# Optimization experiments

Hardware: AMD Instinct MI355X
Metric: run time of the kernel (lower is better)

The kernel has to match this reference:

```python
import jax, jax.numpy as jnp
import numpy as np

D_MODEL = 1024
N_HEADS = 16
D_FF = 512  # FeedForward default d_ff=512 (not overridden in EncoderLayer)
EPS = 1e-6


def _norm(x, alpha, bias):
    # Custom NormLayer: mean + UNBIASED variance (torch.var default, N-1 denom)
    mean = jnp.mean(x, axis=-1, keepdims=True)
    n = x.shape[-1]
    var = jnp.sum((x - mean) ** 2, axis=-1, keepdims=True) / (n - 1)
    return alpha * (x - mean) / jnp.sqrt(var + EPS) + bias


def setup_inputs() -> dict:
    key = jax.random.key(0)
    ks = jax.random.split(key, 12)
    s = 1.0 / np.sqrt(D_MODEL)
    inp = {
        "x": jax.random.normal(ks[0], (2, 2048, D_MODEL), dtype=jnp.float32),
        "Wq": jax.random.uniform(ks[1], (D_MODEL, D_MODEL), jnp.float32, -s, s),
        "bq": jnp.zeros((D_MODEL,), jnp.float32),
        "Wk": jax.random.uniform(ks[2], (D_MODEL, D_MODEL), jnp.float32, -s, s),
        "bk": jnp.zeros((D_MODEL,), jnp.float32),
        "Wv": jax.random.uniform(ks[3], (D_MODEL, D_MODEL), jnp.float32, -s, s),
        "bv": jnp.zeros((D_MODEL,), jnp.float32),
        "Wo": jax.random.uniform(ks[4], (D_MODEL, D_MODEL), jnp.float32, -s, s),
        "bo": jnp.zeros((D_MODEL,), jnp.float32),
        "alpha1": jnp.ones((D_MODEL,), jnp.float32),
        "beta1": jnp.zeros((D_MODEL,), jnp.float32),
        "alpha2": jnp.ones((D_MODEL,), jnp.float32),
        "beta2": jnp.zeros((D_MODEL,), jnp.float32),
        "W1": jax.random.uniform(ks[5], (D_MODEL, D_FF), jnp.float32, -s, s),
        "b1": jnp.zeros((D_FF,), jnp.float32),
        "W2": jax.random.uniform(ks[6], (D_FF, D_MODEL), jnp.float32, -1.0 / np.sqrt(D_FF), 1.0 / np.sqrt(D_FF)),
        "b2": jnp.zeros((D_MODEL,), jnp.float32),
    }
    return inp


def reference(x, Wq, bq, Wk, bk, Wv, bv, Wo, bo, alpha1, beta1, alpha2, beta2, W1, b1, W2, b2):
    B, S, D = x.shape
    H = N_HEADS
    dh = D // H
    # norm_1 applied to x, result feeds BOTH attention and the residual
    x = _norm(x, alpha1, beta1)
    # multihead attention (dropout = identity in eval)
    q = (x @ Wq + bq).reshape(B, S, H, dh)
    k = (x @ Wk + bk).reshape(B, S, H, dh)
    v = (x @ Wv + bv).reshape(B, S, H, dh)
    scores = jnp.einsum("bqhd,bkhd->bhqk", q, k) / jnp.sqrt(jnp.asarray(dh, x.dtype))
    attn = jax.nn.softmax(scores, axis=-1)
    o = jnp.einsum("bhqk,bkhd->bqhd", attn, v).reshape(B, S, D)
    o = o @ Wo + bo
    x = x + o
    # FFN on norm_2(x)
    h = _norm(x, alpha2, beta2)
    h = jax.nn.relu(h @ W1 + b1) @ W2 + b2
    return x + h
```

## Files before the change

### kernel.cpp

```cpp
#include <hip/hip_runtime.h>

typedef __bf16 bf16;
typedef __bf16 bf16x4 __attribute__((ext_vector_type(4)));
typedef __bf16 bf16x8 __attribute__((ext_vector_type(8)));
typedef float f32x4 __attribute__((ext_vector_type(4)));

#define D_MODEL 1024
#define SEQ 2048
#define NB 2
#define LOG2E 1.4426950408889634f

__device__ __forceinline__ void glds16(const bf16* g, bf16* l) {
    __builtin_amdgcn_global_load_lds(
        (const __attribute__((address_space(1))) void*)g,
        (__attribute__((address_space(3))) void*)l, 16, 0, 0);
}

__device__ __forceinline__ void tile_tcvt(
    const float* __restrict__ src, int rows, int cols, bf16* __restrict__ dst,
    int bx, int by, bf16 (*t)[72])
{
    int tid = threadIdx.x;
    int k0 = by * 64, n0 = bx * 64;
    int r = tid >> 2, c = (tid & 3) * 16;
    const float4* s = (const float4*)(src + (size_t)(k0 + r) * cols + n0 + c);
#pragma unroll
    for (int q = 0; q < 4; ++q) {
        float4 v = s[q];
        t[c + q * 4 + 0][r] = (bf16)v.x;
        t[c + q * 4 + 1][r] = (bf16)v.y;
        t[c + q * 4 + 2][r] = (bf16)v.z;
        t[c + q * 4 + 3][r] = (bf16)v.w;
    }
    __syncthreads();
    bf16* d = dst + (size_t)(n0 + r) * rows + k0 + c;
    *(bf16x8*)(d)     = *(const bf16x8*)&t[r][c];
    *(bf16x8*)(d + 8) = *(const bf16x8*)&t[r][c + 8];
}

__global__ __launch_bounds__(256) void prep_kernel(
    const float* __restrict__ Wq, const float* __restrict__ Wk,
    const float* __restrict__ Wv, const float* __restrict__ Wo,
    const float* __restrict__ W1, const float* __restrict__ W2,
    const float* __restrict__ bq, const float* __restrict__ bk,
    const float* __restrict__ bv,
    bf16* __restrict__ Wqkv_t, bf16* __restrict__ Wo_t,
    bf16* __restrict__ W1_t, bf16* __restrict__ W2_t,
    float* __restrict__ b_qkv)
{
    __shared__ bf16 t[64][72];
    int id = blockIdx.x;
    if (id < 1024) {
        int which = id >> 8, tile = id & 255;
        const float* src = which == 0 ? Wq : which == 1 ? Wk : which == 2 ? Wv : Wo;
        bf16* dst = which == 3 ? Wo_t : Wqkv_t + (size_t)which * 1024 * 1024;
        tile_tcvt(src, 1024, 1024, dst, tile & 15, tile >> 4, t);
    } else if (id < 1152) {
        int tile = id - 1024;
        tile_tcvt(W1, 1024, 512, W1_t, tile & 7, tile >> 3, t);
    } else if (id < 1280) {
        int tile = id - 1152;
        tile_tcvt(W2, 512, 1024, W2_t, tile & 15, tile >> 4, t);
    } else {
        int i = (id - 1280) * 256 + threadIdx.x;
        float v;
        if (i < 1024) v = bq[i];
        else if (i < 2048) v = bk[i - 1024];
        else v = bv[i - 2048];
        b_qkv[i] = v;
    }
}

__global__ __launch_bounds__(256) void norm_kernel(
    const float* __restrict__ X, const float* __restrict__ alpha,
    const float* __restrict__ beta, bf16* __restrict__ Y)
{
    int row = blockIdx.x;
    int tid = threadIdx.x;
    float4 v = ((const float4*)(X + (size_t)row * D_MODEL))[tid];
    float s = v.x + v.y + v.z + v.w;
    float ss = v.x*v.x + v.y*v.y + v.z*v.z + v.w*v.w;
#pragma unroll
    for (int off = 1; off < 64; off <<= 1) {
        s  += __shfl_xor(s, off, 64);
        ss += __shfl_xor(ss, off, 64);
    }
    __shared__ float sd[8];
    int wave = tid >> 6, lane = tid & 63;
    if (lane == 0) { sd[wave] = s; sd[4 + wave] = ss; }
    __syncthreads();
    s  = sd[0] + sd[1] + sd[2] + sd[3];
    ss = sd[4] + sd[5] + sd[6] + sd[7];
    float mean = s * (1.0f / 1024.0f);
    float var  = (ss - s * mean) * (1.0f / 1023.0f);
    float rs = rsqrtf(var + 1e-6f);
    float4 a = ((const float4*)alpha)[tid];
    float4 bt = ((const float4*)beta)[tid];
    bf16x4 o;
    o[0] = (bf16)(a.x * (v.x - mean) * rs + bt.x);
    o[1] = (bf16)(a.y * (v.y - mean) * rs + bt.y);
    o[2] = (bf16)(a.z * (v.z - mean) * rs + bt.z);
    o[3] = (bf16)(a.w * (v.w - mean) * rs + bt.w);
    *(bf16x4*)(Y + (size_t)row * D_MODEL + tid * 4) = o;
}

__global__ __launch_bounds__(256) void crelu_kernel(
    const float* __restrict__ p0, const float* __restrict__ p1,
    const float* __restrict__ b1, bf16* __restrict__ h1)
{
    int i = blockIdx.x * 256 + threadIdx.x;
    float4 a = ((const float4*)p0)[i];
    float4 b = ((const float4*)p1)[i];
    int col = (i * 4) & 511;
    float4 bb = *(const float4*)(b1 + col);
    bf16x4 o;
    o[0] = (bf16)fmaxf(a.x + b.x + bb.x, 0.0f);
    o[1] = (bf16)fmaxf(a.y + b.y + bb.y, 0.0f);
    o[2] = (bf16)fmaxf(a.z + b.z + bb.z, 0.0f);
    o[3] = (bf16)fmaxf(a.w + b.w + bb.w, 0.0f);
    ((bf16x4*)h1)[i] = o;
}

template <typename OutT, int BN, int KU, bool VFUSE, bool SPLITK>
__global__ __launch_bounds__(256) void gemm128(
    const bf16* __restrict__ A, const bf16* __restrict__ Bt,
    const float* __restrict__ bias, const bf16* __restrict__ Rb,
    const float* __restrict__ Rf, OutT* __restrict__ C, bf16* __restrict__ vT,
    int M, int N, int K, int lda, int relu)
{
    constexpr int NT = BN / 32;
    constexpr int ASTR = 128 * 32;
    constexpr int BSTR = BN * 32;
    __shared__ bf16 As[ASTR * KU];
    __shared__ bf16 Bs[BSTR * KU];

    int tid = threadIdx.x;
    int wave = tid >> 6, lane = tid & 63;
    int quad = lane >> 4, l16 = lane & 15;
    int m0 = blockIdx.y * 128, n0 = blockIdx.x * BN;
    int wm = (wave >> 1) * 64, wn = (wave & 1) * (BN / 2);
    int Keff = SPLITK ? (K >> 1) : K;
    int klo  = SPLITK ? blockIdx.z * Keff : 0;

    f32x4 acc[4][NT] = {};

    const bf16* ga = A  + (size_t)(m0 + (tid >> 2)) * lda + (tid & 3) * 8 + klo;
    const bf16* gb = Bt + (size_t)(n0 + (tid >> 2)) * K   + (tid & 3) * 8 + klo;
    bf16* lAs = As + wave * 512;
    bf16* lBs = Bs + wave * 512;

    for (int k0 = 0; k0 < Keff; k0 += 32 * KU) {
        __syncthreads();
#pragma unroll
        for (int u = 0; u < KU; ++u) {
            glds16(ga + k0 + u * 32, lAs + u * ASTR);
            glds16(ga + (size_t)64 * lda + k0 + u * 32, lAs + u * ASTR + 2048);
            glds16(gb + k0 + u * 32, lBs + u * BSTR);
            if (BN == 128) glds16(gb + (size_t)64 * K + k0 + u * 32, lBs + u * BSTR + 2048);
        }
        __syncthreads();
#pragma unroll
        for (int u = 0; u < KU; ++u) {
            bf16x8 af[4], bfr[NT];
#pragma unroll
            for (int mt = 0; mt < 4; ++mt)
                af[mt] = *(const bf16x8*)(As + u * ASTR + (wm + mt * 16 + l16) * 32 + quad * 8);
#pragma unroll
            for (int nt = 0; nt < NT; ++nt)
                bfr[nt] = *(const bf16x8*)(Bs + u * BSTR + (wn + nt * 16 + l16) * 32 + quad * 8);
#pragma unroll
            for (int mt = 0; mt < 4; ++mt)
#pragma unroll
                for (int nt = 0; nt < NT; ++nt)
                    acc[mt][nt] = __builtin_amdgcn_mfma_f32_16x16x32_bf16(af[mt], bfr[nt], acc[mt][nt], 0, 0, 0);
        }
    }

    if (SPLITK) {
        float* P = (float*)C + (size_t)blockIdx.z * M * N;
#pragma unroll
        for (int nt = 0; nt < NT; ++nt) {
            int n = n0 + wn + nt * 16 + l16;
#pragma unroll
            for (int mt = 0; mt < 4; ++mt)
#pragma unroll
                for (int r = 0; r < 4; ++r) {
                    int m = m0 + wm + mt * 16 + quad * 4 + r;
                    P[(size_t)m * N + n] = acc[mt][nt][r];
                }
        }
        return;
    }

#pragma unroll
    for (int nt = 0; nt < NT; ++nt) {
        int n = n0 + wn + nt * 16 + l16;
        float bv = bias[n];
        if (VFUSE && n >= 2048) {
            int d = n & 63, h = (n - 2048) >> 6;
#pragma unroll
            for (int mt = 0; mt < 4; ++mt) {
                int m = m0 + wm + mt * 16 + quad * 4;
                int b = m >> 11, sidx = m & 2047;
                bf16x4 pk;
#pragma unroll
                for (int r = 0; r < 4; ++r) pk[r] = (bf16)(acc[mt][nt][r] + bv);
                *(bf16x4*)(vT + (((size_t)(b * 16 + h) * 64 + d) * SEQ + sidx)) = pk;
            }
        } else {
#pragma unroll
            for (int mt = 0; mt < 4; ++mt) {
#pragma unroll
                for (int r = 0; r < 4; ++r) {
                    int m = m0 + wm + mt * 16 + quad * 4 + r;
                    float vv = acc[mt][nt][r] + bv;
                    if (Rb) vv += (float)Rb[(size_t)m * N + n];
                    if (Rf) vv += Rf[(size_t)m * N + n];
                    if (relu) vv = vv > 0.0f ? vv : 0.0f;
                    C[(size_t)m * N + n] = (OutT)vv;
                }
            }
        }
    }
}

__global__ __launch_bounds__(512) void attn_kernel(
    const bf16* __restrict__ qkv, const bf16* __restrict__ vT, bf16* __restrict__ O)
{
    __shared__ __align__(16) char smem[38912];
    bf16* Ks = (bf16*)smem;
    bf16* Vt = (bf16*)(smem + 9216);
    bf16* Ps = (bf16*)(smem + 18432);

    int tid = threadIdx.x;
    int wave = tid >> 6, lane = tid & 63;
    int quad = lane >> 4, l16 = lane & 15;
    int qg = wave >> 1, kg = wave & 1;
    int bh = blockIdx.y, b = bh >> 4, h = bh & 15;
    int q0 = blockIdx.x * 128 + qg * 32;

    const bf16* Qb = qkv + (size_t)(b * SEQ + q0) * 3072 + h * 64;
    const bf16* Kb = qkv + (size_t)(b * SEQ) * 3072 + 1024 + h * 64;
    const bf16* Vb = vT + (size_t)bh * 64 * SEQ;

    const float c_l2 = 0.125f * LOG2E;
    bf16x8 qa[2][2];
#pragma unroll
    for (int mt = 0; mt < 2; ++mt)
#pragma unroll
        for (int hf = 0; hf < 2; ++hf) {
            bf16x8 raw = *(const bf16x8*)(Qb + (size_t)(mt * 16 + l16) * 3072 + hf * 32 + quad * 8);
            bf16x8 sc;
#pragma unroll
            for (int j = 0; j < 8; ++j) sc[j] = (bf16)((float)raw[j] * c_l2);
            qa[mt][hf] = sc;
        }

    float lsum[2] = {};
    f32x4 oacc[2][4] = {};

    int sr = tid >> 3, scol = (tid & 7) * 8;
    const bf16* kp = Kb + (size_t)sr * 3072 + scol;
    const bf16* vp = Vb + (size_t)sr * SEQ + scol;
    bf16x8 kr = *(const bf16x8*)kp;
    bf16x8 vr = *(const bf16x8*)vp;

    bf16* PsW = Ps + wave * 32 * 40;
    const bf16* KsKg = Ks + kg * 32 * 72;

    for (int kt = 0; kt < SEQ; kt += 64) {
        __syncthreads();
        *(bf16x8*)(Ks + sr * 72 + scol) = kr;
        *(bf16x8*)(Vt + sr * 72 + scol) = vr;
        __syncthreads();
        if (kt + 64 < SEQ) {
            kr = *(const bf16x8*)(kp + (size_t)(kt + 64) * 3072);
            vr = *(const bf16x8*)(vp + kt + 64);
        }

        bf16x8 kb[2][2], vb[4];
#pragma unroll
        for (int t4 = 0; t4 < 2; ++t4) {
            kb[t4][0] = *(const bf16x8*)(KsKg + (t4 * 16 + l16) * 72 + quad * 8);
            kb[t4][1] = *(const bf16x8*)(KsKg + (t4 * 16 + l16) * 72 + 32 + quad * 8);
        }
#pragma unroll
        for (int dt = 0; dt < 4; ++dt)
            vb[dt] = *(const bf16x8*)(Vt + (dt * 16 + l16) * 72 + kg * 32 + quad * 8);

#pragma unroll
        for (int mt = 0; mt < 2; ++mt)
#pragma unroll
            for (int t4 = 0; t4 < 2; ++t4) {
                f32x4 c = {};
                c = __builtin_amdgcn_mfma_f32_16x16x32_bf16(kb[t4][0], qa[mt][0], c, 0, 0, 0);
                c = __builtin_amdgcn_mfma_f32_16x16x32_bf16(kb[t4][1], qa[mt][1], c, 0, 0, 0);
                bf16x4 pk;
                float psum = 0.0f;
#pragma unroll
                for (int r = 0; r < 4; ++r) {
                    float p = exp2f(c[r]);
                    psum += p;
                    pk[r] = (bf16)p;
                }
                lsum[mt] += psum;
                *(bf16x4*)(PsW + (mt * 16 + l16) * 40 + t4 * 16 + quad * 4) = pk;
            }
#pragma unroll
        for (int mt = 0; mt < 2; ++mt) {
            bf16x8 pa = *(const bf16x8*)(PsW + (mt * 16 + l16) * 40 + quad * 8);
#pragma unroll
            for (int dt = 0; dt < 4; ++dt)
                oacc[mt][dt] = __builtin_amdgcn_mfma_f32_16x16x32_bf16(pa, vb[dt], oacc[mt][dt], 0, 0, 0);
        }
    }

    float lr[2];
#pragma unroll
    for (int mt = 0; mt < 2; ++mt) {
        lr[mt] = lsum[mt];
        lr[mt] += __shfl_xor(lr[mt], 16);
        lr[mt] += __shfl_xor(lr[mt], 32);
    }
    __syncthreads();
    float* sf = (float*)smem;
    float* lb = sf + 8192;
    if (kg == 1) {
#pragma unroll
        for (int mt = 0; mt < 2; ++mt)
#pragma unroll
            for (int dt = 0; dt < 4; ++dt)
                *(f32x4*)&sf[qg * 2048 + (dt * 16 + l16) * 32 + mt * 16 + quad * 4] = oacc[mt][dt];
        if (lane < 16) {
            lb[(qg * 2 + 0) * 16 + l16] = lr[0];
            lb[(qg * 2 + 1) * 16 + l16] = lr[1];
        }
    }
    __syncthreads();
    if (kg == 0) {
#pragma unroll
        for (int mt = 0; mt < 2; ++mt) {
            lr[mt] += lb[(qg * 2 + mt) * 16 + l16];
#pragma unroll
            for (int dt = 0; dt < 4; ++dt) {
                f32x4 other = *(const f32x4*)&sf[qg * 2048 + (dt * 16 + l16) * 32 + mt * 16 + quad * 4];
                oacc[mt][dt] += other;
            }
        }
#pragma unroll
        for (int mt = 0; mt < 2; ++mt)
#pragma unroll
            for (int r = 0; r < 4; ++r) {
                float inv = 1.0f / __shfl(lr[mt], quad * 4 + r, 16);
                int row = b * SEQ + q0 + mt * 16 + quad * 4 + r;
                bf16* op = O + (size_t)row * D_MODEL + h * 64;
#pragma unroll
                for (int dt = 0; dt < 4; ++dt)
                    op[dt * 16 + l16] = (bf16)(oacc[mt][dt][r] * inv);
            }
    }
}

extern "C" void kernel_launch(void* const* d_in, const int* in_sizes, int n_in,
                              void* d_out, int out_size, void* d_ws, size_t ws_size,
                              hipStream_t stream)
{
    const float* x      = (const float*)d_in[0];
    const float* Wq     = (const float*)d_in[1];
    const float* bq     = (const float*)d_in[2];
    const float* Wk     = (const float*)d_in[3];
    const float* bk     = (const float*)d_in[4];
    const float* Wv     = (const float*)d_in[5];
    const float* bv     = (const float*)d_in[6];
    const float* Wo     = (const float*)d_in[7];
    const float* bo     = (const float*)d_in[8];
    const float* alpha1 = (const float*)d_in[9];
    const float* beta1  = (const float*)d_in[10];
    const float* alpha2 = (const float*)d_in[11];
    const float* beta2  = (const float*)d_in[12];
    const float* W1     = (const float*)d_in[13];
    const float* b1     = (const float*)d_in[14];
    const float* W2     = (const float*)d_in[15];
    const float* b2     = (const float*)d_in[16];

    char* ws = (char*)d_ws;
    const size_t MB = 1ull << 20;
    bf16*  Wqkv_t = (bf16*)(ws + 0 * MB);
    bf16*  Wo_t   = (bf16*)(ws + 6 * MB);
    bf16*  W1_t   = (bf16*)(ws + 8 * MB);
    bf16*  W2_t   = (bf16*)(ws + 9 * MB);
    float* b_qkv  = (float*)(ws + 10 * MB);
    bf16*  xn     = (bf16*)(ws + 11 * MB);
    bf16*  qkv    = (bf16*)(ws + 19 * MB);
    bf16*  vT     = (bf16*)(ws + 43 * MB);
    bf16*  o      = (bf16*)(ws + 51 * MB);
    float* x2     = (float*)(ws + 19 * MB);
    bf16*  hn     = (bf16*)(ws + 35 * MB);
    float* pF1    = (float*)(ws + 43 * MB);
    bf16*  h1     = (bf16*)(ws + 11 * MB);

    const int M = NB * SEQ;

    prep_kernel<<<1292, 256, 0, stream>>>(Wq, Wk, Wv, Wo, W1, W2, bq, bk, bv,
                                          Wqkv_t, Wo_t, W1_t, W2_t, b_qkv);

    norm_kernel<<<M, 256, 0, stream>>>(x, alpha1, beta1, xn);

    gemm128<bf16, 128, 2, true, false><<<dim3(24, 32), 256, 0, stream>>>(
        xn, Wqkv_t, b_qkv, nullptr, nullptr, qkv, vT, M, 3072, D_MODEL, D_MODEL, 0);

    attn_kernel<<<dim3(SEQ / 128, 32), 512, 0, stream>>>(qkv, vT, o);

    gemm128<float, 64, 2, false, false><<<dim3(16, 32), 256, 0, stream>>>(
        o, Wo_t, bo, xn, nullptr, x2, nullptr, M, D_MODEL, D_MODEL, D_MODEL, 0);

    norm_kernel<<<M, 256, 0, stream>>>(x2, alpha2, beta2, hn);

    gemm128<float, 64, 2, false, true><<<dim3(8, 32, 2), 256, 0, stream>>>(
        hn, W1_t, nullptr, nullptr, nullptr, pF1, nullptr, M, 512, D_MODEL, D_MODEL, 0);

    crelu_kernel<<<(M * 512) / 1024, 256, 0, stream>>>(
        pF1, pF1 + (size_t)M * 512, b1, h1);

    gemm128<float, 64, 2, false, false><<<dim3(16, 32), 256, 0, stream>>>(
        h1, W2_t, b2, nullptr, x2, (float*)d_out, nullptr, M, D_MODEL, 512, 512, 0);
}
```

Before: 269.1 us.

## Merge first norm into prep kernel and widen attention key tiles to 128

The first layer norm is folded into the weight-prep launch, with extra blocks so one kernel launch is removed. The attention kernel now processes 128 keys per iteration instead of 64, halving the barrier count. V fragments are read directly from global memory into registers instead of being staged through shared memory. The risks are higher register pressure and uncoalesced or uncached global V reads in the inner loop, and the Ps buffer is larger.

After: 306.6 us. +14.0%, slower.

```diff
diff --git a/kernel.cpp b/kernel.cpp
--- a/kernel.cpp
+++ b/kernel.cpp
@@ -38,7 +38,41 @@
     *(bf16x8*)(d + 8) = *(const bf16x8*)&t[r][c + 8];
 }
 
-__global__ __launch_bounds__(256) void prep_kernel(
+__device__ __forceinline__ void norm_row(
+    const float* __restrict__ X, const float* __restrict__ alpha,
+    const float* __restrict__ beta, bf16* __restrict__ Y, int row)
+{
+    int tid = threadIdx.x;
+    float4 v = ((const float4*)(X + (size_t)row * D_MODEL))[tid];
+    float s = v.x + v.y + v.z + v.w;
+    float ss = v.x*v.x + v.y*v.y + v.z*v.z + v.w*v.w;
+#pragma unroll
+    for (int off = 1; off < 64; off <<= 1) {
+        s  += __shfl_xor(s, off, 64);
+        ss += __shfl_xor(ss, off, 64);
+    }
+    __shared__ float sd[8];
+    int wave = tid >> 6, lane = tid & 63;
+    if (lane == 0) { sd[wave] = s; sd[4 + wave] = ss; }
+    __syncthreads();
+    s  = sd[0] + sd[1] + sd[2] + sd[3];
+    ss = sd[4] + sd[5] + sd[6] + sd[7];
+    float mean = s * (1.0f / 1024.0f);
+    float var  = (ss - s * mean) * (1.0f / 1023.0f);
+    float rs = rsqrtf(var + 1e-6f);
+    float4 a = ((const float4*)alpha)[tid];
+    float4 bt = ((const float4*)beta)[tid];
+    bf16x4 o;
+    o[0] = (bf16)(a.x * (v.x - mean) * rs + bt.x);
+    o[1] = (bf16)(a.y * (v.y - mean) * rs + bt.y);
+    o[2] = (bf16)(a.z * (v.z - mean) * rs + bt.z);
+    o[3] = (bf16)(a.w * (v.w - mean) * rs + bt.w);
+    *(bf16x4*)(Y + (size_t)row * D_MODEL + tid * 4) = o;
+}
+
+__global__ __launch_bounds__(256) void prep_norm_kernel(
+    const float* __restrict__ x, const float* __restrict__ alpha1,
+    const float* __restrict__ beta1, bf16* __restrict__ xn,
     const float* __restrict__ Wq, const float* __restrict__ Wk,
     const float* __restrict__ Wv, const float* __restrict__ Wo,
     const float* __restrict__ W1, const float* __restrict__ W2,
@@ -50,6 +84,11 @@
 {
     __shared__ bf16 t[64][72];
     int id = blockIdx.x;
+    if (id < 4096) {
+        norm_row(x, alpha1, beta1, xn, id);
+        return;
+    }
+    id -= 4096;
     if (id < 1024) {
         int which = id >> 8, tile = id & 255;
         const float* src = which == 0 ? Wq : which == 1 ? Wk : which == 2 ? Wv : Wo;
@@ -75,33 +114,7 @@
     const float* __restrict__ X, const float* __restrict__ alpha,
     const float* __restrict__ beta, bf16* __restrict__ Y)
 {
-    int row = blockIdx.x;
-    int tid = threadIdx.x;
-    float4 v = ((const float4*)(X + (size_t)row * D_MODEL))[tid];
-    float s = v.x + v.y + v.z + v.w;
-    float ss = v.x*v.x + v.y*v.y + v.z*v.z + v.w*v.w;
-#pragma unroll
-    for (int off = 1; off < 64; off <<= 1) {
-        s  += __shfl_xor(s, off, 64);
-        ss += __shfl_xor(ss, off, 64);
-    }
-    __shared__ float sd[8];
-    int wave = tid >> 6, lane = tid & 63;
-    if (lane == 0) { sd[wave] = s; sd[4 + wave] = ss; }
-    __syncthreads();
-    s  = sd[0] + sd[1] + sd[2] + sd[3];
-    ss = sd[4] + sd[5] + sd[6] + sd[7];
-    float mean = s * (1.0f / 1024.0f);
-    float var  = (ss - s * mean) * (1.0f / 1023.0f);
-    float rs = rsqrtf(var + 1e-6f);
-    float4 a = ((const float4*)alpha)[tid];
-    float4 bt = ((const float4*)beta)[tid];
-    bf16x4 o;
-    o[0] = (bf16)(a.x * (v.x - mean) * rs + bt.x);
-    o[1] = (bf16)(a.y * (v.y - mean) * rs + bt.y);
-    o[2] = (bf16)(a.z * (v.z - mean) * rs + bt.z);
-    o[3] = (bf16)(a.w * (v.w - mean) * rs + bt.w);
-    *(bf16x4*)(Y + (size_t)row * D_MODEL + tid * 4) = o;
+    norm_row(X, alpha, beta, Y, blockIdx.x);
 }
 
 __global__ __launch_bounds__(256) void crelu_kernel(
@@ -227,10 +240,8 @@
 __global__ __launch_bounds__(512) void attn_kernel(
     const bf16* __restrict__ qkv, const bf16* __restrict__ vT, bf16* __restrict__ O)
 {
-    __shared__ __align__(16) char smem[38912];
-    bf16* Ks = (bf16*)smem;
-    bf16* Vt = (bf16*)(smem + 9216);
-    bf16* Ps = (bf16*)(smem + 18432);
+    __shared__ bf16 Ks[128][72];
+    __shared__ bf16 Ps[8][32][72];
 
     int tid = threadIdx.x;
     int wave = tid >> 6, lane = tid & 63;
@@ -259,39 +270,45 @@
     float lsum[2] = {};
     f32x4 oacc[2][4] = {};
 
-    int sr = tid >> 3, scol = (tid & 7) * 8;
+    int sr = tid >> 2, scol = (tid & 3) * 16;
     const bf16* kp = Kb + (size_t)sr * 3072 + scol;
-    const bf16* vp = Vb + (size_t)sr * SEQ + scol;
-    bf16x8 kr = *(const bf16x8*)kp;
-    bf16x8 vr = *(const bf16x8*)vp;
-
-    bf16* PsW = Ps + wave * 32 * 40;
-    const bf16* KsKg = Ks + kg * 32 * 72;
-
-    for (int kt = 0; kt < SEQ; kt += 64) {
+    bf16x8 kr0 = ((const bf16x8*)kp)[0];
+    bf16x8 kr1 = ((const bf16x8*)kp)[1];
+
+    bf16* PsW = &Ps[wave][0][0];
+    const bf16* KsKg = &Ks[kg * 64][0];
+    const bf16* vrow = Vb + (size_t)l16 * SEQ + kg * 64 + quad * 8;
+
+    for (int kt = 0; kt < SEQ; kt += 128) {
         __syncthreads();
-        *(bf16x8*)(Ks + sr * 72 + scol) = kr;
-        *(bf16x8*)(Vt + sr * 72 + scol) = vr;
+        *(bf16x8*)&Ks[sr][scol]     = kr0;
+        *(bf16x8*)&Ks[sr][scol + 8] = kr1;
         __syncthreads();
-        if (kt + 64 < SEQ) {
-            kr = *(const bf16x8*)(kp + (size_t)(kt + 64) * 3072);
-            vr = *(const bf16x8*)(vp + kt + 64);
-        }
-
-        bf16x8 kb[2][2], vb[4];
-#pragma unroll
-        for (int t4 = 0; t4 < 2; ++t4) {
+        if (kt + 128 < SEQ) {
+            const bf16* kn = kp + (size_t)(kt + 128) * 3072;
+            kr0 = ((const bf16x8*)kn)[0];
+            kr1 = ((const bf16x8*)kn)[1];
+        }
+
+        bf16x8 vb[4][2];
+#pragma unroll
+        for (int dt = 0; dt < 4; ++dt) {
+            const bf16* vp = vrow + (size_t)dt * 16 * SEQ + kt;
+            vb[dt][0] = *(const bf16x8*)(vp);
+            vb[dt][1] = *(const bf16x8*)(vp + 32);
+        }
+
+        bf16x8 kb[4][2];
+#pragma unroll
+        for (int t4 = 0; t4 < 4; ++t4) {
             kb[t4][0] = *(const bf16x8*)(KsKg + (t4 * 16 + l16) * 72 + quad * 8);
             kb[t4][1] = *(const bf16x8*)(KsKg + (t4 * 16 + l16) * 72 + 32 + quad * 8);
         }
-#pragma unroll
-        for (int dt = 0; dt < 4; ++dt)
-            vb[dt] = *(const bf16x8*)(Vt + (dt * 16 + l16) * 72 + kg * 32 + quad * 8);
 
 #pragma unroll
         for (int mt = 0; mt < 2; ++mt)
 #pragma unroll
-            for (int t4 = 0; t4 < 2; ++t4) {
+            for (int t4 = 0; t4 < 4; ++t4) {
                 f32x4 c = {};
                 c = __builtin_amdgcn_mfma_f32_16x16x32_bf16(kb[t4][0], qa[mt][0], c, 0, 0, 0);
                 c = __builtin_amdgcn_mfma_f32_16x16x32_bf16(kb[t4][1], qa[mt][1], c, 0, 0, 0);
@@ -304,14 +321,17 @@
                     pk[r] = (bf16)p;
                 }
                 lsum[mt] += psum;
-                *(bf16x4*)(PsW + (mt * 16 + l16) * 40 + t4 * 16 + quad * 4) = pk;
+                *(bf16x4*)(PsW + (mt * 16 + l16) * 72 + t4 * 16 + quad * 4) = pk;
             }
 #pragma unroll
         for (int mt = 0; mt < 2; ++mt) {
-            bf16x8 pa = *(const bf16x8*)(PsW + (mt * 16 + l16) * 40 + quad * 8);
-#pragma unroll
-            for (int dt = 0; dt < 4; ++dt)
-                oacc[mt][dt] = __builtin_amdgcn_mfma_f32_16x16x32_bf16(pa, vb[dt], oacc[mt][dt], 0, 0, 0);
+            bf16x8 pa0 = *(const bf16x8*)(PsW + (mt * 16 + l16) * 72 + quad * 8);
+            bf16x8 pa1 = *(const bf16x8*)(PsW + (mt * 16 + l16) * 72 + 32 + quad * 8);
+#pragma unroll
+            for (int dt = 0; dt < 4; ++dt) {
+                oacc[mt][dt] = __builtin_amdgcn_mfma_f32_16x16x32_bf16(pa0, vb[dt][0], oacc[mt][dt], 0, 0, 0);
+                oacc[mt][dt] = __builtin_amdgcn_mfma_f32_16x16x32_bf16(pa1, vb[dt][1], oacc[mt][dt], 0, 0, 0);
+            }
         }
     }
 
@@ -323,8 +343,8 @@
         lr[mt] += __shfl_xor(lr[mt], 32);
     }
     __syncthreads();
-    float* sf = (float*)smem;
-    float* lb = sf + 8192;
+    float* sf = (float*)&Ps[0][0][0];
+    float* lb = (float*)&Ks[0][0];
     if (kg == 1) {
 #pragma unroll
         for (int mt = 0; mt < 2; ++mt)
@@ -401,10 +421,9 @@
 
     const int M = NB * SEQ;
 
-    prep_kernel<<<1292, 256, 0, stream>>>(Wq, Wk, Wv, Wo, W1, W2, bq, bk, bv,
-                                          Wqkv_t, Wo_t, W1_t, W2_t, b_qkv);
-
-    norm_kernel<<<M, 256, 0, stream>>>(x, alpha1, beta1, xn);
+    prep_norm_kernel<<<4096 + 1292, 256, 0, stream>>>(
+        x, alpha1, beta1, xn, Wq, Wk, Wv, Wo, W1, W2, bq, bk, bv,
+        Wqkv_t, Wo_t, W1_t, W2_t, b_qkv);
 
     gemm128<bf16, 128, 2, true, false><<<dim3(24, 32), 256, 0, stream>>>(
         xn, Wqkv_t, b_qkv, nullptr, nullptr, qkv, vT, M, 3072, D_MODEL, D_MODEL, 0);
```

## Fuse first norm into prep kernel and drop split-K FFN1 with relu epilogue

Applied to the files above, without the earlier changes.

Merges the weight transpose/convert prep kernel and the first layer norm into one launch, with the first 4096 blocks doing norm rows. Replaces the split-K FFN1 GEMM plus its separate combine/ReLU kernel with a single non-split GEMM that applies bias and ReLU in its epilogue and writes bf16 directly. This removes two launches and the fp32 partial-sum round trip through memory. In exchange the FFN1 GEMM runs only 256 blocks, which lowers parallelism on a large GPU, and the prep kernel's shared memory now also holds the norm scratch.

Result: no change. 271.9 us (+1.1%).

```diff
diff --git a/kernel.cpp b/kernel.cpp
--- a/kernel.cpp
+++ b/kernel.cpp
@@ -38,7 +38,41 @@
     *(bf16x8*)(d + 8) = *(const bf16x8*)&t[r][c + 8];
 }
 
-__global__ __launch_bounds__(256) void prep_kernel(
+__device__ __forceinline__ void norm_row(
+    const float* __restrict__ X, const float* __restrict__ alpha,
+    const float* __restrict__ beta, bf16* __restrict__ Y, int row)
+{
+    int tid = threadIdx.x;
+    float4 v = ((const float4*)(X + (size_t)row * D_MODEL))[tid];
+    float s = v.x + v.y + v.z + v.w;
+    float ss = v.x*v.x + v.y*v.y + v.z*v.z + v.w*v.w;
+#pragma unroll
+    for (int off = 1; off < 64; off <<= 1) {
+        s  += __shfl_xor(s, off, 64);
+        ss += __shfl_xor(ss, off, 64);
+    }
+    __shared__ float sd[8];
+    int wave = tid >> 6, lane = tid & 63;
+    if (lane == 0) { sd[wave] = s; sd[4 + wave] = ss; }
+    __syncthreads();
+    s  = sd[0] + sd[1] + sd[2] + sd[3];
+    ss = sd[4] + sd[5] + sd[6] + sd[7];
+    float mean = s * (1.0f / 1024.0f);
+    float var  = (ss - s * mean) * (1.0f / 1023.0f);
+    float rs = rsqrtf(var + 1e-6f);
+    float4 a = ((const float4*)alpha)[tid];
+    float4 bt = ((const float4*)beta)[tid];
+    bf16x4 o;
+    o[0] = (bf16)(a.x * (v.x - mean) * rs + bt.x);
+    o[1] = (bf16)(a.y * (v.y - mean) * rs + bt.y);
+    o[2] = (bf16)(a.z * (v.z - mean) * rs + bt.z);
+    o[3] = (bf16)(a.w * (v.w - mean) * rs + bt.w);
+    *(bf16x4*)(Y + (size_t)row * D_MODEL + tid * 4) = o;
+}
+
+__global__ __launch_bounds__(256) void prep_norm_kernel(
+    const float* __restrict__ x, const float* __restrict__ alpha1,
+    const float* __restrict__ beta1, bf16* __restrict__ xn,
     const float* __restrict__ Wq, const float* __restrict__ Wk,
     const float* __restrict__ Wv, const float* __restrict__ Wo,
     const float* __restrict__ W1, const float* __restrict__ W2,
@@ -50,6 +84,11 @@
 {
     __shared__ bf16 t[64][72];
     int id = blockIdx.x;
+    if (id < 4096) {
+        norm_row(x, alpha1, beta1, xn, id);
+        return;
+    }
+    id -= 4096;
     if (id < 1024) {
         int which = id >> 8, tile = id & 255;
         const float* src = which == 0 ? Wq : which == 1 ? Wk : which == 2 ? Wv : Wo;
@@ -75,53 +114,10 @@
     const float* __restrict__ X, const float* __restrict__ alpha,
     const float* __restrict__ beta, bf16* __restrict__ Y)
 {
-    int row = blockIdx.x;
-    int tid = threadIdx.x;
-    float4 v = ((const float4*)(X + (size_t)row * D_MODEL))[tid];
-    float s = v.x + v.y + v.z + v.w;
-    float ss = v.x*v.x + v.y*v.y + v.z*v.z + v.w*v.w;
-#pragma unroll
-    for (int off = 1; off < 64; off <<= 1) {
-        s  += __shfl_xor(s, off, 64);
-        ss += __shfl_xor(ss, off, 64);
-    }
-    __shared__ float sd[8];
-    int wave = tid >> 6, lane = tid & 63;
-    if (lane == 0) { sd[wave] = s; sd[4 + wave] = ss; }
-    __syncthreads();
-    s  = sd[0] + sd[1] + sd[2] + sd[3];
-    ss = sd[4] + sd[5] + sd[6] + sd[7];
-    float mean = s * (1.0f / 1024.0f);
-    float var  = (ss - s * mean) * (1.0f / 1023.0f);
-    float rs = rsqrtf(var + 1e-6f);
-    float4 a = ((const float4*)alpha)[tid];
-    float4 bt = ((const float4*)beta)[tid];
-    bf16x4 o;
-    o[0] = (bf16)(a.x * (v.x - mean) * rs + bt.x);
-    o[1] = (bf16)(a.y * (v.y - mean) * rs + bt.y);
-    o[2] = (bf16)(a.z * (v.z - mean) * rs + bt.z);
-    o[3] = (bf16)(a.w * (v.w - mean) * rs + bt.w);
-    *(bf16x4*)(Y + (size_t)row * D_MODEL + tid * 4) = o;
-}
-
-__global__ __launch_bounds__(256) void crelu_kernel(
-    const float* __restrict__ p0, const float* __restrict__ p1,
-    const float* __restrict__ b1, bf16* __restrict__ h1)
-{
-    int i = blockIdx.x * 256 + threadIdx.x;
-    float4 a = ((const float4*)p0)[i];
-    float4 b = ((const float4*)p1)[i];
-    int col = (i * 4) & 511;
-    float4 bb = *(const float4*)(b1 + col);
-    bf16x4 o;
-    o[0] = (bf16)fmaxf(a.x + b.x + bb.x, 0.0f);
-    o[1] = (bf16)fmaxf(a.y + b.y + bb.y, 0.0f);
-    o[2] = (bf16)fmaxf(a.z + b.z + bb.z, 0.0f);
-    o[3] = (bf16)fmaxf(a.w + b.w + bb.w, 0.0f);
-    ((bf16x4*)h1)[i] = o;
-}
-
-template <typename OutT, int BN, int KU, bool VFUSE, bool SPLITK>
+    norm_row(X, alpha, beta, Y, blockIdx.x);
+}
+
+template <typename OutT, int BN, int KU, bool VFUSE>
 __global__ __launch_bounds__(256) void gemm128(
     const bf16* __restrict__ A, const bf16* __restrict__ Bt,
     const float* __restrict__ bias, const bf16* __restrict__ Rb,
@@ -139,17 +135,15 @@
     int quad = lane >> 4, l16 = lane & 15;
     int m0 = blockIdx.y * 128, n0 = blockIdx.x * BN;
     int wm = (wave >> 1) * 64, wn = (wave & 1) * (BN / 2);
-    int Keff = SPLITK ? (K >> 1) : K;
-    int klo  = SPLITK ? blockIdx.z * Keff : 0;
 
     f32x4 acc[4][NT] = {};
 
-    const bf16* ga = A  + (size_t)(m0 + (tid >> 2)) * lda + (tid & 3) * 8 + klo;
-    const bf16* gb = Bt + (size_t)(n0 + (tid >> 2)) * K   + (tid & 3) * 8 + klo;
+    const bf16* ga = A  + (size_t)(m0 + (tid >> 2)) * lda + (tid & 3) * 8;
+    const bf16* gb = Bt + (size_t)(n0 + (tid >> 2)) * K   + (tid & 3) * 8;
     bf16* lAs = As + wave * 512;
     bf16* lBs = Bs + wave * 512;
 
-    for (int k0 = 0; k0 < Keff; k0 += 32 * KU) {
+    for (int k0 = 0; k0 < K; k0 += 32 * KU) {
         __syncthreads();
 #pragma unroll
         for (int u = 0; u < KU; ++u) {
@@ -174,22 +168,6 @@
                 for (int nt = 0; nt < NT; ++nt)
                     acc[mt][nt] = __builtin_amdgcn_mfma_f32_16x16x32_bf16(af[mt], bfr[nt], acc[mt][nt], 0, 0, 0);
         }
-    }
-
-    if (SPLITK) {
-        float* P = (float*)C + (size_t)blockIdx.z * M * N;
-#pragma unroll
-        for (int nt = 0; nt < NT; ++nt) {
-            int n = n0 + wn + nt * 16 + l16;
-#pragma unroll
-            for (int mt = 0; mt < 4; ++mt)
-#pragma unroll
-                for (int r = 0; r < 4; ++r) {
-                    int m = m0 + wm + mt * 16 + quad * 4 + r;
-                    P[(size_t)m * N + n] = acc[mt][nt][r];
-                }
-        }
-        return;
     }
 
 #pragma unroll
@@ -396,32 +374,27 @@
     bf16*  o      = (bf16*)(ws + 51 * MB);
     float* x2     = (float*)(ws + 19 * MB);
     bf16*  hn     = (bf16*)(ws + 35 * MB);
-    float* pF1    = (float*)(ws + 43 * MB);
     bf16*  h1     = (bf16*)(ws + 11 * MB);
 
     const int M = NB * SEQ;
 
-    prep_kernel<<<1292, 256, 0, stream>>>(Wq, Wk, Wv, Wo, W1, W2, bq, bk, bv,
-                                          Wqkv_t, Wo_t, W1_t, W2_t, b_qkv);
-
-    norm_kernel<<<M, 256, 0, stream>>>(x, alpha1, beta1, xn);
-
-    gemm128<bf16, 128, 2, true, false><<<dim3(24, 32), 256, 0, stream>>>(
+    prep_norm_kernel<<<4096 + 1292, 256, 0, stream>>>(
+        x, alpha1, beta1, xn, Wq, Wk, Wv, Wo, W1, W2, bq, bk, bv,
+        Wqkv_t, Wo_t, W1_t, W2_t, b_qkv);
+
+    gemm128<bf16, 128, 2, true><<<dim3(24, 32), 256, 0, stream>>>(
         xn, Wqkv_t, b_qkv, nullptr, nullptr, qkv, vT, M, 3072, D_MODEL, D_MODEL, 0);
 
     attn_kernel<<<dim3(SEQ / 128, 32), 512, 0, stream>>>(qkv, vT, o);
 
-    gemm128<float, 64, 2, false, false><<<dim3(16, 32), 256, 0, stream>>>(
+    gemm128<float, 64, 2, false><<<dim3(16, 32), 256, 0, stream>>>(
         o, Wo_t, bo, xn, nullptr, x2, nullptr, M, D_MODEL, D_MODEL, D_MODEL, 0);
 
     norm_kernel<<<M, 256, 0, stream>>>(x2, alpha2, beta2, hn);
 
-    gemm128<float, 64, 2, false, true><<<dim3(8, 32, 2), 256, 0, stream>>>(
-        hn, W1_t, nullptr, nullptr, nullptr, pF1, nullptr, M, 512, D_MODEL, D_MODEL, 0);
-
-    crelu_kernel<<<(M * 512) / 1024, 256, 0, stream>>>(
-        pF1, pF1 + (size_t)M * 512, b1, h1);
-
-    gemm128<float, 64, 2, false, false><<<dim3(16, 32), 256, 0, stream>>>(
+    gemm128<bf16, 64, 2, false><<<dim3(8, 32), 256, 0, stream>>>(
+        hn, W1_t, b1, nullptr, nullptr, h1, nullptr, M, 512, D_MODEL, D_MODEL, 1);
+
+    gemm128<float, 64, 2, false><<<dim3(16, 32), 256, 0, stream>>>(
         h1, W2_t, b2, nullptr, x2, (float*)d_out, nullptr, M, D_MODEL, 512, 512, 0);
 }
```
